# Kernel optimization log

Measured on AMD Instinct MI355X. Metric: run time of the kernel, lower is better.

## Reference

```python
import jax, jax.numpy as jnp
import numpy as np

LMAX, MMAX = 6, 2
C, COUT = 128, 128
M_SIZE = [LMAX - m + 1 for m in range(MMAX + 1)]  # [7, 6, 5]
LN_EPS = 1e-5


def _perm():
    # l-primary layout (input): for l in 0..lmax, m in -min(l,mmax)..min(l,mmax)
    lp = [(l, m) for l in range(LMAX + 1) for m in range(-min(l, MMAX), min(l, MMAX) + 1)]
    # m-primary layout (CoefficientMapping.to_m): m=0 block, then per m: real(+m) block, imag(-m) block
    mp = [(l, 0) for l in range(LMAX + 1)]
    for m in range(1, MMAX + 1):
        mp += [(l, m) for l in range(m, LMAX + 1)]
        mp += [(l, -m) for l in range(m, LMAX + 1)]
    return np.array([lp.index(t) for t in mp], dtype=np.int32)

PERM = _perm()  # length 29


def setup_inputs() -> dict:
    key = jax.random.key(0)
    ks = jax.random.split(key, 8)
    E = 30000
    num_coeff = sum(2 * min(l, MMAX) + 1 for l in range(LMAX + 1))  # 29
    rad_out = C * sum(M_SIZE)  # 2304 = num_channels_rad
    s = 0.02
    return {
        "x_emb": jax.random.normal(ks[0], (E, num_coeff, C), jnp.float32),
        "x_edge": jax.random.normal(ks[1], (E, C), jnp.float32),
        # RadialFunction: Linear(C,C)+LN+SiLU, Linear(C, rad_out)
        "rad_w1": jax.random.normal(ks[2], (C, C), jnp.float32) * s,
        "rad_b1": jnp.zeros((C,), jnp.float32),
        "rad_g": jnp.ones((C,), jnp.float32),
        "rad_beta": jnp.zeros((C,), jnp.float32),
        "rad_w2": jax.random.normal(ks[3], (rad_out, C), jnp.float32) * s,
        "rad_b2": jnp.ones((rad_out,), jnp.float32),  # gate ~1 so signal survives
        # fc_m0: Linear(7*C, COUT*7, bias=True)
        "w_m0": jax.random.normal(ks[4], (M_SIZE[0] * COUT, M_SIZE[0] * C), jnp.float32) * s,
        "b_m0": jnp.zeros((M_SIZE[0] * COUT,), jnp.float32),
        # SO2_m_Convolution fc for m=1,2: Linear(msz*C, 2*COUT*msz, bias=False)
        "w_m1": jax.random.normal(ks[5], (2 * COUT * M_SIZE[1], M_SIZE[1] * C), jnp.float32) * s,
        "w_m2": jax.random.normal(ks[6], (2 * COUT * M_SIZE[2], M_SIZE[2] * C), jnp.float32) * s,
    }


def reference(x_emb, x_edge, rad_w1, rad_b1, rad_g, rad_beta, rad_w2, rad_b2,
              w_m0, b_m0, w_m1, w_m2):
    E = x_emb.shape[0]
    # _m_primary: permute coefficients from l-primary to m-primary layout
    xm = x_emb[:, PERM, :]  # (E, 29, C)

    # RadialFunction: Linear + LayerNorm + SiLU + Linear
    h = x_edge @ rad_w1.T + rad_b1
    mu = jnp.mean(h, axis=-1, keepdims=True)
    var = jnp.var(h, axis=-1, keepdims=True)
    h = (h - mu) * jax.lax.rsqrt(var + LN_EPS) * rad_g + rad_beta
    h = jax.nn.silu(h)
    rad = h @ rad_w2.T + rad_b2  # (E, 2304)

    # m = 0
    m0 = M_SIZE[0]
    x0 = xm[:, :m0, :].reshape(E, m0 * C)
    x0 = x0 * rad[:, : m0 * C]
    x0 = x0 @ w_m0.T + b_m0  # (E, m0*COUT)
    outs = [x0.reshape(E, m0, COUT)]

    offset, offr = m0, m0 * C
    for msz, w in zip(M_SIZE[1:], (w_m1, w_m2)):
        # (E, 2, msz*C): row 0 = real(+m) coeffs, row 1 = imag(-m) coeffs
        x_m = xm[:, offset:offset + 2 * msz, :].reshape(E, 2, msz * C)
        x_m = x_m * rad[:, offr:offr + msz * C][:, None, :]
        y = jnp.einsum('eki,oi->eko', x_m, w)  # (E, 2, 2*COUT*msz)
        half = w.shape[0] // 2
        y_r, y_i = y[..., :half], y[..., half:]
        out_r = y_r[:, 0:1] - y_i[:, 1:2]
        out_i = y_r[:, 1:2] + y_i[:, 0:1]
        outs.append(jnp.concatenate([out_r, out_i], axis=1).reshape(E, 2 * msz, COUT))
        offset += 2 * msz
        offr += msz * C

    return jnp.concatenate(outs, axis=1)  # (E, 29, COUT), m-primary layout
```

## Files before the change

kernel.cpp:

```cpp
#include <hip/hip_runtime.h>
#include <stdint.h>

typedef unsigned short u16;
typedef __attribute__((ext_vector_type(8))) short short8;
typedef __attribute__((ext_vector_type(8))) u16 u16x8;
typedef __attribute__((ext_vector_type(4))) u16 u16x4;
typedef __attribute__((ext_vector_type(4))) float f32x4;

#define E_TOT 30000
#define TL    3712

__constant__ int d_PERM[29] = {0,2,6,11,16,21,26, 3,7,12,17,22,27, 1,5,10,15,20,25,
                               8,13,18,23,28, 4,9,14,19,24};
__constant__ int d_RINV[18][2] = {
  {0,-1},{1,-1},{2,-1},{3,-1},{4,-1},{5,-1},{6,-1},
  {7,13},{8,14},{9,15},{10,16},{11,17},{12,18},
  {19,24},{20,25},{21,26},{22,27},{23,28}};

__device__ __forceinline__ u16 f2bf(float f){
  union { float f; uint32_t u; } v; v.f = f;
  return (u16)((v.u + 0x7FFFu + ((v.u >> 16) & 1u)) >> 16);
}
__device__ __forceinline__ float bf2f(u16 u){
  union { uint32_t u; float f; } v; v.u = ((uint32_t)u) << 16;
  return v.f;
}
__device__ __forceinline__ void gl_lds16(const void* g, void* l){
  __builtin_amdgcn_global_load_lds((const __attribute__((address_space(1))) void*)g,
                                   (__attribute__((address_space(3))) void*)l, 16, 0, 0);
}

__global__ void k_build_w(const float* __restrict__ w0, const float* __restrict__ w1,
                          const float* __restrict__ w2, const float* __restrict__ rw2,
                          u16* __restrict__ W0, u16* __restrict__ W1, u16* __restrict__ W2,
                          u16* __restrict__ w2b){
  int idx = blockIdx.x * 256 + threadIdx.x;
  if (idx < 2304*128){ w2b[idx] = f2bf(rw2[idx]); return; }
  idx -= 2304*128;
  if (idx < 1024*896){
    W0[idx] = (idx < 896*896) ? f2bf(w0[idx]) : (u16)0;
    return;
  }
  idx -= 1024*896;
  if (idx < 1536*1536){
    const int half = 768;
    int o = idx / 1536, i2 = idx - o*1536;
    float v;
    if (o < half) v = (i2 < half) ? w1[o*half + i2] : -w1[(half+o)*half + (i2-half)];
    else { int op = o - half;
           v = (i2 < half) ? w1[(half+op)*half + i2] : w1[op*half + (i2-half)]; }
    W1[idx] = f2bf(v);
    return;
  }
  idx -= 1536*1536;
  if (idx < 1280*1280){
    const int half = 640;
    int o = idx / 1280, i2 = idx - o*1280;
    float v;
    if (o < half) v = (i2 < half) ? w2[o*half + i2] : -w2[(half+o)*half + (i2-half)];
    else { int op = o - half;
           v = (i2 < half) ? w2[(half+op)*half + i2] : w2[op*half + (i2-half)]; }
    W2[idx] = f2bf(v);
  }
}

__global__ __launch_bounds__(256) void k_h(const float* __restrict__ xe,
    const float* __restrict__ w1, const float* __restrict__ b1,
    const float* __restrict__ g, const float* __restrict__ beta,
    u16* __restrict__ hout){
  __shared__ float sw[128*132];
  __shared__ float sxe[16*128];
  int tid = threadIdx.x;
  #pragma unroll
  for (int q = 0; q < 16; q++){
    int i4 = q*256 + tid;
    int row = i4 >> 5, c4 = (i4 & 31) * 4;
    *(f32x4*)&sw[row*132 + c4] = *(const f32x4*)&w1[row*128 + c4];
  }
  int el = tid >> 4, s = tid & 15;
  for (int g8 = 0; g8 < 8; g8++){
    long eb = (long)blockIdx.x * 128 + g8*16;
    if (eb >= E_TOT) break;
    __syncthreads();
    #pragma unroll
    for (int q = 0; q < 2; q++){
      int off = q*1024 + tid*4;
      long er = eb + (off >> 7); if (er > (long)(E_TOT-1)) er = (long)(E_TOT-1);
      *(f32x4*)&sxe[off] = *(const f32x4*)&xe[er*128 + (off & 127)];
    }
    __syncthreads();
    float acc[8];
    #pragma unroll
    for (int q = 0; q < 8; q++) acc[q] = 0.f;
    const float* xr = &sxe[el*128];
    for (int c4 = 0; c4 < 32; c4++){
      f32x4 x = *(const f32x4*)&xr[c4*4];
      #pragma unroll
      for (int q = 0; q < 8; q++){
        f32x4 w = *(const f32x4*)&sw[(s + 16*q)*132 + c4*4];
        acc[q] += x[0]*w[0] + x[1]*w[1] + x[2]*w[2] + x[3]*w[3];
      }
    }
    float sum = 0.f, ss = 0.f;
    #pragma unroll
    for (int q = 0; q < 8; q++){
      acc[q] += b1[s + 16*q];
      sum += acc[q]; ss += acc[q]*acc[q];
    }
    #pragma unroll
    for (int m = 1; m < 16; m <<= 1){ sum += __shfl_xor(sum, m); ss += __shfl_xor(ss, m); }
    float mu = sum * (1.f/128.f);
    float var = ss * (1.f/128.f) - mu*mu;
    float rs = rsqrtf(var + 1e-5f);
    long e = eb + el;
    if (e < (long)E_TOT){
      #pragma unroll
      for (int q = 0; q < 8; q++){
        int j = s + 16*q;
        float v = (acc[q] - mu) * rs * g[j] + beta[j];
        v = v / (1.f + expf(-v));
        hout[e*128 + j] = f2bf(v);
      }
    }
  }
}

__global__ __launch_bounds__(256) void k_radt(
    const u16* __restrict__ h, const u16* __restrict__ w2b,
    const float* __restrict__ b2, const float* __restrict__ xemb,
    u16* __restrict__ t)
{
  __shared__ u16 sH[64*136];
  __shared__ u16 sT[2][64*72];
  int tid = threadIdx.x;
  long eb = (long)blockIdx.x * 64;
  int nn0 = blockIdx.y * 9;
  #pragma unroll
  for (int q = 0; q < 4; q++){
    int ch = q*256 + tid;
    int row = ch >> 4, col = (ch & 15) * 8;
    long er = eb + row; if (er > (long)(E_TOT-1)) er = (long)(E_TOT-1);
    *(u16x8*)&sH[row*136 + col] = *(const u16x8*)&h[er*128 + col];
  }
  __syncthreads();
  int lane = tid & 63, wid = tid >> 6;
  int wr = wid >> 1, wc = wid & 1;
  int lr = lane & 15, lh = lane >> 4;
  short8 afr[2][4];
  #pragma unroll
  for (int mi = 0; mi < 2; mi++)
    #pragma unroll
    for (int ks = 0; ks < 4; ks++)
      afr[mi][ks] = *(const short8*)&sH[(wr*32 + mi*16 + lr)*136 + ks*32 + lh*8];

  for (int nn = nn0; nn < nn0 + 9; ++nn){
    int p = nn & 1;
    int nb = nn * 64;
    f32x4 acc[2][2];
    #pragma unroll
    for (int mi = 0; mi < 2; mi++)
      #pragma unroll
      for (int nj = 0; nj < 2; nj++){ acc[mi][nj][0]=0;acc[mi][nj][1]=0;acc[mi][nj][2]=0;acc[mi][nj][3]=0; }
    #pragma unroll
    for (int ks = 0; ks < 4; ks++){
      #pragma unroll
      for (int nj = 0; nj < 2; nj++){
        short8 bf = *(const short8*)&w2b[(long)(nb + wc*32 + nj*16 + lr)*128 + ks*32 + lh*8];
        #pragma unroll
        for (int mi = 0; mi < 2; mi++)
          acc[mi][nj] = __builtin_amdgcn_mfma_f32_16x16x32_bf16(afr[mi][ks], bf, acc[mi][nj], 0, 0, 0);
      }
    }
    int rcb = nb >> 7, chalf = nb & 64;
    int nr = (d_RINV[rcb][1] >= 0) ? 2 : 1;
    f32x4 px0[2][2], px1[2][2];
    #pragma unroll
    for (int rr = 0; rr < 2; rr++){
      if (rr < nr){
        int xrow = d_PERM[d_RINV[rcb][rr]];
        #pragma unroll
        for (int q = 0; q < 2; q++){
          int ch = q*256 + tid;
          int row = ch >> 3, c8 = (ch & 7) * 8;
          long e = eb + row;
          if (e < (long)E_TOT){
            const float* xp = &xemb[(e*29 + xrow)*128 + chalf + c8];
            px0[rr][q] = *(const f32x4*)xp;
            px1[rr][q] = *(const f32x4*)(xp + 4);
          }
        }
      }
    }
    #pragma unroll
    for (int mi = 0; mi < 2; mi++){
      #pragma unroll
      for (int nj = 0; nj < 2; nj++){
        int col = wc*32 + nj*16 + lr;
        float bv = b2[nb + col];
        #pragma unroll
        for (int q = 0; q < 4; q++){
          int row = wr*32 + mi*16 + lh*4 + q;
          sT[p][row*72 + col] = f2bf(acc[mi][nj][q] + bv);
        }
      }
    }
    __syncthreads();
    #pragma unroll
    for (int rr = 0; rr < 2; rr++){
      if (rr < nr){
        int r = d_RINV[rcb][rr];
        #pragma unroll
        for (int q = 0; q < 2; q++){
          int ch = q*256 + tid;
          int row = ch >> 3, c8 = (ch & 7) * 8;
          long e = eb + row;
          if (e < (long)E_TOT){
            u16x8 rv = *(const u16x8*)&sT[p][row*72 + c8];
            u16x8 o;
            o[0]=f2bf(px0[rr][q][0]*bf2f(rv[0])); o[1]=f2bf(px0[rr][q][1]*bf2f(rv[1]));
            o[2]=f2bf(px0[rr][q][2]*bf2f(rv[2])); o[3]=f2bf(px0[rr][q][3]*bf2f(rv[3]));
            o[4]=f2bf(px1[rr][q][0]*bf2f(rv[4])); o[5]=f2bf(px1[rr][q][1]*bf2f(rv[5]));
            o[6]=f2bf(px1[rr][q][2]*bf2f(rv[6])); o[7]=f2bf(px1[rr][q][3]*bf2f(rv[7]));
            *(u16x8*)&t[(e*29 + r)*128 + chalf + c8] = o;
          }
        }
      }
    }
  }
}

__global__ __launch_bounds__(512, 4) void k_gemm(
    const u16* __restrict__ A,
    const u16* __restrict__ W0c, const u16* __restrict__ W1c, const u16* __restrict__ W2c,
    const float* __restrict__ bias0, float* __restrict__ out)
{
  __shared__ u16 S[24576];

  int orig = blockIdx.x;
  int xcd = orig & 7, idxs = orig >> 3;
  int wgid = (xcd < 6 ? xcd*428 : 2568 + (xcd-6)*427) + idxs;

  int mi_ = wgid / 29, nidx = wgid - mi_*29;
  int mrow = mi_ * 256;
  int K, kbase, ncol, nvalid; const u16* Wg; const float* bias = nullptr;
  if (nidx < 12)      { K=1536; kbase=896;  Wg=W1c; ncol=nidx*128;      nvalid=1536; }
  else if (nidx < 22) { K=1280; kbase=2432; Wg=W2c; ncol=(nidx-12)*128; nvalid=1280; }
  else                { K=896;  kbase=0;    Wg=W0c; ncol=(nidx-22)*128; nvalid=896; bias=bias0; }
  int nkt = K >> 6;

  int tid = threadIdx.x;
  int lane = tid & 63, wid = tid >> 6;
  int wr = wid >> 1, wc = wid & 1;
  int lr = lane & 15, lh = lane >> 4;
  int swz = (lane & 7) << 3;

  const u16* gsrc[6]; int ldso[6];
  #pragma unroll
  for (int q = 0; q < 4; q++){
    int CH = q*512 + tid;
    int row = CH >> 3, c16 = CH & 7;
    long e = mrow + row; if (e > (long)(E_TOT-1)) e = (long)(E_TOT-1);
    gsrc[q] = A + e*(long)TL + kbase + ((c16 ^ (row & 7)) << 3);
    ldso[q] = row*64 + c16*8;
  }
  #pragma unroll
  for (int q = 0; q < 2; q++){
    int CH = q*512 + tid;
    int row = CH >> 3, c16 = CH & 7;
    gsrc[4+q] = Wg + (long)(ncol + row)*K + ((c16 ^ (row & 7)) << 3);
    ldso[4+q] = 16384 + row*64 + c16*8;
  }

  f32x4 acc[4][4];
  #pragma unroll
  for (int i = 0; i < 4; i++)
    #pragma unroll
    for (int j = 0; j < 4; j++){ acc[i][j][0]=0;acc[i][j][1]=0;acc[i][j][2]=0;acc[i][j][3]=0; }

  for (int t = 0; t < nkt; ++t){
    if (t) __syncthreads();
    #pragma unroll
    for (int q = 0; q < 6; q++){ gl_lds16(gsrc[q], &S[ldso[q]]); gsrc[q] += 64; }
    __syncthreads();
    short8 af[4][2];
    #pragma unroll
    for (int i = 0; i < 4; i++)
      #pragma unroll
      for (int ks = 0; ks < 2; ks++)
        af[i][ks] = *(const short8*)&S[(wr*64 + i*16 + lr)*64 + ((ks*32 + lh*8) ^ swz)];
    #pragma unroll
    for (int nj = 0; nj < 4; nj++){
      short8 bf[2];
      #pragma unroll
      for (int ks = 0; ks < 2; ks++)
        bf[ks] = *(const short8*)&S[16384 + (wc*64 + nj*16 + lr)*64 + ((ks*32 + lh*8) ^ swz)];
      #pragma unroll
      for (int ks = 0; ks < 2; ks++)
        #pragma unroll
        for (int i = 0; i < 4; i++)
          acc[i][nj] = __builtin_amdgcn_mfma_f32_16x16x32_bf16(af[i][ks], bf[ks], acc[i][nj], 0, 0, 0);
    }
  }

  #pragma unroll
  for (int i = 0; i < 4; i++){
    #pragma unroll
    for (int j = 0; j < 4; j++){
      int col = wc*64 + j*16 + lr;
      if (ncol + col < nvalid){
        float bv = bias ? bias[ncol + col] : 0.f;
        #pragma unroll
        for (int q = 0; q < 4; q++){
          long row = mrow + wr*64 + i*16 + lh*4 + q;
          if (row < E_TOT)
            out[row*(long)TL + kbase + ncol + col] = acc[i][j][q] + bv;
        }
      }
    }
  }
}

extern "C" void kernel_launch(void* const* d_in, const int* in_sizes, int n_in,
                              void* d_out, int out_size, void* d_ws, size_t ws_size,
                              hipStream_t stream){
  (void)in_sizes; (void)n_in; (void)out_size;
  const float* x_emb  = (const float*)d_in[0];
  const float* x_edge = (const float*)d_in[1];
  const float* rad_w1 = (const float*)d_in[2];
  const float* rad_b1 = (const float*)d_in[3];
  const float* rad_g  = (const float*)d_in[4];
  const float* rad_bt = (const float*)d_in[5];
  const float* rad_w2 = (const float*)d_in[6];
  const float* rad_b2 = (const float*)d_in[7];
  const float* w_m0   = (const float*)d_in[8];
  const float* b_m0   = (const float*)d_in[9];
  const float* w_m1   = (const float*)d_in[10];
  const float* w_m2   = (const float*)d_in[11];
  float* out = (float*)d_out;
  char* ws = (char*)d_ws;

  u16* t   = (u16*)(ws + 0);
  u16* h   = (u16*)(ws + 222720000);
  u16* W0  = (u16*)(ws + 230400000);
  u16* W1  = (u16*)(ws + 232235008);
  u16* W2  = (u16*)(ws + 236953600);
  u16* w2b = (u16*)(ws + 240230400);
  if (ws_size < 240820224ull) return;

  k_build_w<<<dim3(20352), dim3(256), 0, stream>>>(w_m0, w_m1, w_m2, rad_w2,
                                                   W0, W1, W2, w2b);
  k_h<<<dim3(235), dim3(256), 0, stream>>>(x_edge, rad_w1, rad_b1, rad_g, rad_bt, h);
  k_radt<<<dim3(469, 4), dim3(256), 0, stream>>>(h, w2b, rad_b2, x_emb, t);
  k_gemm<<<dim3(3422), dim3(512), 0, stream>>>(t, W0, W1, W2, b_m0, out);
}
```

Measured before the change: 647.4 us.

## Triple-buffer GEMM LDS with ping-pong wave groups; regrid radial kernel

```diff
diff --git a/kernel.cpp b/kernel.cpp
--- a/kernel.cpp
+++ b/kernel.cpp
@@ -134,7 +134,7 @@
   __shared__ u16 sT[2][64*72];
   int tid = threadIdx.x;
   long eb = (long)blockIdx.x * 64;
-  int nn0 = blockIdx.y * 9;
+  int nn0 = blockIdx.y * 4;
   #pragma unroll
   for (int q = 0; q < 4; q++){
     int ch = q*256 + tid;
@@ -153,7 +153,7 @@
     for (int ks = 0; ks < 4; ks++)
       afr[mi][ks] = *(const short8*)&sH[(wr*32 + mi*16 + lr)*136 + ks*32 + lh*8];
 
-  for (int nn = nn0; nn < nn0 + 9; ++nn){
+  for (int nn = nn0; nn < nn0 + 4; ++nn){
     int p = nn & 1;
     int nb = nn * 64;
     f32x4 acc[2][2];
@@ -229,12 +229,53 @@
   }
 }
 
-__global__ __launch_bounds__(512, 4) void k_gemm(
+#define WVM6 asm volatile("s_waitcnt vmcnt(6)" ::: "memory");
+#define WVM0 asm volatile("s_waitcnt vmcnt(0)" ::: "memory");
+#define LGK0 asm volatile("s_waitcnt lgkmcnt(0)" ::: "memory");
+#define BARR __builtin_amdgcn_s_barrier();
+
+#define STAGE(bufc)                                                           \
+  { _Pragma("unroll")                                                         \
+    for (int q = 0; q < 6; q++){                                              \
+      gl_lds16(gsrc[q], S0 + (bufc)*24576 + ldso[q]);                         \
+      gsrc[q] += 64;                                                          \
+    } }
+
+#define READT(bufc)                                                           \
+  _Pragma("unroll")                                                           \
+  for (int i = 0; i < 4; i++){                                                \
+    _Pragma("unroll")                                                         \
+    for (int ks = 0; ks < 2; ks++)                                            \
+      af[i][ks] = *(const short8*)&S0[(bufc)*24576 +                          \
+                    (wr*64 + i*16 + lr)*64 + ((ks*32 + lh*8) ^ swz)];         \
+  }                                                                           \
+  _Pragma("unroll")                                                           \
+  for (int j = 0; j < 4; j++){                                                \
+    _Pragma("unroll")                                                         \
+    for (int ks = 0; ks < 2; ks++)                                            \
+      bfr[j][ks] = *(const short8*)&S0[(bufc)*24576 + 16384 +                 \
+                    (wc*64 + j*16 + lr)*64 + ((ks*32 + lh*8) ^ swz)];         \
+  }
+
+#define MFMA32                                                                \
+  __builtin_amdgcn_s_setprio(1);                                              \
+  _Pragma("unroll")                                                           \
+  for (int ks = 0; ks < 2; ks++)                                              \
+    _Pragma("unroll")                                                         \
+    for (int i = 0; i < 4; i++)                                               \
+      _Pragma("unroll")                                                       \
+      for (int j = 0; j < 4; j++)                                             \
+        acc[i][j] = __builtin_amdgcn_mfma_f32_16x16x32_bf16(                  \
+            af[i][ks], bfr[j][ks], acc[i][j], 0, 0, 0);                       \
+  __builtin_amdgcn_s_setprio(0);
+
+__global__ __launch_bounds__(512, 2) void k_gemm(
     const u16* __restrict__ A,
     const u16* __restrict__ W0c, const u16* __restrict__ W1c, const u16* __restrict__ W2c,
     const float* __restrict__ bias0, float* __restrict__ out)
 {
-  __shared__ u16 S[24576];
+  __shared__ u16 S[3][24576];
+  u16* S0 = &S[0][0];
 
   int orig = blockIdx.x;
   int xcd = orig & 7, idxs = orig >> 3;
@@ -250,7 +291,7 @@
 
   int tid = threadIdx.x;
   int lane = tid & 63, wid = tid >> 6;
-  int wr = wid >> 1, wc = wid & 1;
+  int wr = wid & 3, wc = wid >> 2;
   int lr = lane & 15, lh = lane >> 4;
   int swz = (lane & 7) << 3;
 
@@ -277,30 +318,36 @@
     #pragma unroll
     for (int j = 0; j < 4; j++){ acc[i][j][0]=0;acc[i][j][1]=0;acc[i][j][2]=0;acc[i][j][3]=0; }
 
+  short8 af[4][2];
+  short8 bfr[4][2];
+
+  STAGE(0)
+  STAGE(1)
+  WVM6
+  BARR
+
+  int bc = 0;
+  int bs = 2;
   for (int t = 0; t < nkt; ++t){
-    if (t) __syncthreads();
-    #pragma unroll
-    for (int q = 0; q < 6; q++){ gl_lds16(gsrc[q], &S[ldso[q]]); gsrc[q] += 64; }
-    __syncthreads();
-    short8 af[4][2];
-    #pragma unroll
-    for (int i = 0; i < 4; i++)
-      #pragma unroll
-      for (int ks = 0; ks < 2; ks++)
-        af[i][ks] = *(const short8*)&S[(wr*64 + i*16 + lr)*64 + ((ks*32 + lh*8) ^ swz)];
-    #pragma unroll
-    for (int nj = 0; nj < 4; nj++){
-      short8 bf[2];
-      #pragma unroll
-      for (int ks = 0; ks < 2; ks++)
-        bf[ks] = *(const short8*)&S[16384 + (wc*64 + nj*16 + lr)*64 + ((ks*32 + lh*8) ^ swz)];
-      #pragma unroll
-      for (int ks = 0; ks < 2; ks++)
-        #pragma unroll
-        for (int i = 0; i < 4; i++)
-          acc[i][nj] = __builtin_amdgcn_mfma_f32_16x16x32_bf16(af[i][ks], bf[ks], acc[i][nj], 0, 0, 0);
-    }
-  }
+    if (wid < 4){
+      READT(bc)
+      MFMA32
+    } else {
+      if (t > 0) { MFMA32 }
+      READT(bc)
+    }
+    if (t + 2 < nkt){
+      STAGE(bs)
+      WVM6
+    } else if (t + 2 == nkt){
+      WVM0
+    }
+    LGK0
+    BARR
+    bc = (bc == 2) ? 0 : bc + 1;
+    bs = (bs == 2) ? 0 : bs + 1;
+  }
+  if (wid >= 4){ MFMA32 }
 
   #pragma unroll
   for (int i = 0; i < 4; i++){
@@ -350,6 +397,6 @@
   k_build_w<<<dim3(20352), dim3(256), 0, stream>>>(w_m0, w_m1, w_m2, rad_w2,
                                                    W0, W1, W2, w2b);
   k_h<<<dim3(235), dim3(256), 0, stream>>>(x_edge, rad_w1, rad_b1, rad_g, rad_bt, h);
-  k_radt<<<dim3(469, 4), dim3(256), 0, stream>>>(h, w2b, rad_b2, x_emb, t);
+  k_radt<<<dim3(469, 9), dim3(256), 0, stream>>>(h, w2b, rad_b2, x_emb, t);
   k_gemm<<<dim3(3422), dim3(512), 0, stream>>>(t, W0, W1, W2, b_m0, out);
 }
```

Measured after the change: 646.7 us. Within noise of the previous version (-0.1%).
